# Kernel optimization log

Hardware: AMD Instinct MI355X
Metric: run time of the kernel (lower is better)

The kernel has to match this reference:

```python
import jax, jax.numpy as jnp
import numpy as np

K_RET = 10  # top-K retrieved sources per instance


def _pointnet(pts, W1, b1, W2, b2, W3, b3, Wf, bf):
    # pts: [B, P, 3] -> per-point MLP, max-pool over points, final fc -> [B, 256]
    h = jax.nn.relu(pts @ W1 + b1)
    h = jax.nn.relu(h @ W2 + b2)
    h = jax.nn.relu(h @ W3 + b3)
    g = jnp.max(h, axis=1)
    return g @ Wf + bf


def setup_inputs() -> dict:
    key = jax.random.key(0)
    ks = iter(jax.random.split(key, 48))
    B, H, W = 64, 32, 32
    S, D, PL, NPART, NPAR, PSRC = 1024, 256, 32, 16, 96, 512
    s = 0.02

    def w(shape):
        return jax.random.normal(next(ks), shape, jnp.float32) * s

    inp = {"noc_points": jax.random.normal(next(ks), (B, 3, H, W), jnp.float32)}
    # two PointNet-style encoders: target_encoder (te_) and retrieval_encoder (re_)
    for pfx in ("te", "re"):
        inp[pfx + "_W1"] = w((3, 64)); inp[pfx + "_b1"] = jnp.zeros((64,), jnp.float32)
        inp[pfx + "_W2"] = w((64, 128)); inp[pfx + "_b2"] = jnp.zeros((128,), jnp.float32)
        inp[pfx + "_W3"] = w((128, D)); inp[pfx + "_b3"] = jnp.zeros((D,), jnp.float32)
        inp[pfx + "_Wf"] = w((D, D)); inp[pfx + "_bf"] = jnp.zeros((D,), jnp.float32)
    # ParamDecoder2: input 256+256+32 = 544 -> 256 -> 256 -> 6
    inp["dec_W1"] = w((D + D + PL, 256)); inp["dec_b1"] = jnp.zeros((256,), jnp.float32)
    inp["dec_W2"] = w((256, 256)); inp["dec_b2"] = jnp.zeros((256,), jnp.float32)
    inp["dec_W3"] = w((256, 6)); inp["dec_b3"] = jnp.zeros((6,), jnp.float32)
    # precomputed source banks
    inp["ret_src_codes"] = jax.random.normal(next(ks), (S, D), jnp.float32)
    inp["src_codes"] = jax.random.normal(next(ks), (S, D), jnp.float32)
    inp["src_variances"] = jax.random.uniform(next(ks), (S, D), jnp.float32)
    inp["part_latent"] = w((S, NPART, PL))
    inp["def_param"] = w((S, NPAR))
    inp["proj_mat"] = w((S, NPAR, NPAR))        # constraint projection per source
    inp["mat"] = w((S, 3 * PSRC, NPAR))         # points_mat per source
    return inp


def reference(noc_points, te_W1, te_b1, te_W2, te_b2, te_W3, te_b3, te_Wf, te_bf,
              re_W1, re_b1, re_W2, re_b2, re_W3, re_b3, re_Wf, re_bf,
              dec_W1, dec_b1, dec_W2, dec_b2, dec_W3, dec_b3,
              ret_src_codes, src_codes, src_variances, part_latent,
              def_param, proj_mat, mat):
    B = noc_points.shape[0]
    pts = noc_points.reshape(B, 3, -1).transpose(0, 2, 1)        # [B, P, 3]
    tgt = _pointnet(pts, te_W1, te_b1, te_W2, te_b2, te_W3, te_b3, te_Wf, te_bf)  # [B, 256]
    ret = _pointnet(pts, re_W1, re_b1, re_W2, re_b2, re_W3, re_b3, re_Wf, re_bf)  # [B, 256]
    # variance-weighted squared distance to every source latent code
    d = jnp.sum(src_variances[None] * (ret[:, None, :] - ret_src_codes[None]) ** 2, axis=-1)  # [B, S]
    _, idx = jax.lax.top_k(-d, K_RET)                            # [B, K]
    NPART = part_latent.shape[1]
    src_lat = src_codes[idx]                                     # [B, K, 256]
    parts = part_latent[idx]                                     # [B, K, NPART, 32]
    tgt_b = jnp.broadcast_to(tgt[:, None, None, :], (B, K_RET, NPART, tgt.shape[-1]))
    src_b = jnp.broadcast_to(src_lat[:, :, None, :], (B, K_RET, NPART, src_lat.shape[-1]))
    x = jnp.concatenate([tgt_b, src_b, parts], axis=-1)          # [B, K, NPART, 544]
    h = jax.nn.relu(x @ dec_W1 + dec_b1)
    h = jax.nn.relu(h @ dec_W2 + dec_b2)
    raw = (h @ dec_W3 + dec_b3).reshape(B, K_RET, -1)            # [B, K, 96]
    params = jnp.einsum('bkij,bkj->bki', proj_mat[idx], raw) + def_param[idx]  # [B, K, 96]
    pts_def = jnp.einsum('bkpj,bkj->bkp', mat[idx], params)      # [B, K, 3*PSRC]
    psrc = mat.shape[1] // 3
    return pts_def.reshape(B, K_RET, psrc, 3)
```

## Files before the change

### kernel.cpp

```cpp
#include <hip/hip_runtime.h>
#include <cstdint>
#include <cstddef>


#define NB    64
#define NPTS  1024
#define NSRC  1024
#define DIM   256
#define KRET  10
#define NPART 16
#define PL    32
#define NPAR  96
#define P3    1536

__global__ __launch_bounds__(256) void pointnet_kernel(
    const float* __restrict__ noc,
    const float* __restrict__ te_W1, const float* __restrict__ te_b1,
    const float* __restrict__ te_W2, const float* __restrict__ te_b2,
    const float* __restrict__ te_W3, const float* __restrict__ te_b3,
    const float* __restrict__ re_W1, const float* __restrict__ re_b1,
    const float* __restrict__ re_W2, const float* __restrict__ re_b2,
    const float* __restrict__ re_W3, const float* __restrict__ re_b3,
    float* __restrict__ g)
{
  const int chunk = blockIdx.x;
  const int b     = blockIdx.y;
  const int e     = blockIdx.z;

  const float* W1 = e ? re_W1 : te_W1;  const float* b1 = e ? re_b1 : te_b1;
  const float* W2 = e ? re_W2 : te_W2;  const float* b2 = e ? re_b2 : te_b2;
  const float* W3 = e ? re_W3 : te_W3;  const float* b3 = e ? re_b3 : te_b3;

  __shared__ __align__(16) float h1L[64][72];
  __shared__ __align__(16) float h2L[64][132];

  const int t = threadIdx.x;

  {
    const int p = t & 63;
    const int w = t >> 6;
    const float p0 = noc[(b*3 + 0)*NPTS + chunk*64 + p];
    const float p1 = noc[(b*3 + 1)*NPTS + chunk*64 + p];
    const float p2 = noc[(b*3 + 2)*NPTS + chunk*64 + p];
    #pragma unroll
    for (int kk = 0; kk < 16; ++kk) {
      const int k = w*16 + kk;
      float v = b1[k] + p0*W1[0*64 + k] + p1*W1[1*64 + k] + p2*W1[2*64 + k];
      h1L[p][k] = fmaxf(v, 0.f);
    }
  }
  __syncthreads();

  {
    const int tp = t >> 5;
    const int tj = t & 31;
    float acc[8][4];
    #pragma unroll
    for (int pp = 0; pp < 8; ++pp)
      #pragma unroll
      for (int jj = 0; jj < 4; ++jj) acc[pp][jj] = 0.f;

    for (int k = 0; k < 64; k += 4) {
      float4 a[8];
      #pragma unroll
      for (int pp = 0; pp < 8; ++pp)
        a[pp] = *(const float4*)&h1L[tp*8 + pp][k];
      float4 w[4];
      #pragma unroll
      for (int kk = 0; kk < 4; ++kk)
        w[kk] = *(const float4*)&W2[(k + kk)*128 + tj*4];
      #pragma unroll
      for (int pp = 0; pp < 8; ++pp) {
        const float* av = (const float*)&a[pp];
        #pragma unroll
        for (int kk = 0; kk < 4; ++kk) {
          const float* wv = (const float*)&w[kk];
          #pragma unroll
          for (int jj = 0; jj < 4; ++jj)
            acc[pp][jj] += av[kk] * wv[jj];
        }
      }
    }
    float4 bv = *(const float4*)&b2[tj*4];
    const float* bvv = (const float*)&bv;
    #pragma unroll
    for (int pp = 0; pp < 8; ++pp) {
      float4 r;
      float* rv = (float*)&r;
      #pragma unroll
      for (int jj = 0; jj < 4; ++jj)
        rv[jj] = fmaxf(acc[pp][jj] + bvv[jj], 0.f);
      *(float4*)&h2L[tp*8 + pp][tj*4] = r;
    }
  }
  __syncthreads();

  {
    const int tp = t >> 5;
    const int tj = t & 31;
    float acc[8][8];
    #pragma unroll
    for (int pp = 0; pp < 8; ++pp)
      #pragma unroll
      for (int jj = 0; jj < 8; ++jj) acc[pp][jj] = 0.f;

    for (int k = 0; k < 128; k += 4) {
      float4 a[8];
      #pragma unroll
      for (int pp = 0; pp < 8; ++pp)
        a[pp] = *(const float4*)&h2L[tp*8 + pp][k];
      float4 w0[4], w1[4];
      #pragma unroll
      for (int kk = 0; kk < 4; ++kk) {
        w0[kk] = *(const float4*)&W3[(k + kk)*256 + tj*8];
        w1[kk] = *(const float4*)&W3[(k + kk)*256 + tj*8 + 4];
      }
      #pragma unroll
      for (int pp = 0; pp < 8; ++pp) {
        const float* av = (const float*)&a[pp];
        #pragma unroll
        for (int kk = 0; kk < 4; ++kk) {
          const float* wa = (const float*)&w0[kk];
          const float* wb = (const float*)&w1[kk];
          #pragma unroll
          for (int jj = 0; jj < 4; ++jj) {
            acc[pp][jj]     += av[kk] * wa[jj];
            acc[pp][jj + 4] += av[kk] * wb[jj];
          }
        }
      }
    }

    float bb[8];
    {
      float4 b3a = *(const float4*)&b3[tj*8];
      float4 b3b = *(const float4*)&b3[tj*8 + 4];
      const float* xa = (const float*)&b3a;
      const float* xb = (const float*)&b3b;
      #pragma unroll
      for (int jj = 0; jj < 4; ++jj) { bb[jj] = xa[jj]; bb[jj+4] = xb[jj]; }
    }
    float m[8];
    #pragma unroll
    for (int jj = 0; jj < 8; ++jj) {
      float mx = 0.f;
      #pragma unroll
      for (int pp = 0; pp < 8; ++pp)
        mx = fmaxf(mx, fmaxf(acc[pp][jj] + bb[jj], 0.f));
      m[jj] = mx;
    }

    float* redL = &h1L[0][0];
    {
      float4 r0, r1;
      float* a0 = (float*)&r0; float* a1 = (float*)&r1;
      #pragma unroll
      for (int jj = 0; jj < 4; ++jj) { a0[jj] = m[jj]; a1[jj] = m[jj+4]; }
      *(float4*)&redL[tp*260 + tj*8]     = r0;
      *(float4*)&redL[tp*260 + tj*8 + 4] = r1;
    }
    __syncthreads();
    {
      float mx = redL[t];
      #pragma unroll
      for (int q = 1; q < 8; ++q) mx = fmaxf(mx, redL[q*260 + t]);
      atomicMax((int*)&g[(e*NB + b)*DIM + t], __float_as_int(mx));
    }
  }
}

__global__ __launch_bounds__(256) void fc_kernel(
    const float* __restrict__ g,
    const float* __restrict__ te_Wf, const float* __restrict__ te_bf,
    const float* __restrict__ re_Wf, const float* __restrict__ re_bf,
    float* __restrict__ enc)
{
  const int be = blockIdx.x;
  const int e = be >> 6, b = be & 63;
  const float* Wf = e ? re_Wf : te_Wf;
  const float* bf = e ? re_bf : te_bf;
  __shared__ __align__(16) float gL[256];
  const int t = threadIdx.x;
  gL[t] = g[(e*NB + b)*DIM + t];
  __syncthreads();
  float acc = bf[t];
  #pragma unroll 4
  for (int i = 0; i < 256; ++i)
    acc += gL[i] * Wf[i*256 + t];
  enc[(e*NB + b)*DIM + t] = acc;
}

__global__ __launch_bounds__(256) void topk_kernel(
    const float* __restrict__ enc,
    const float* __restrict__ var,
    const float* __restrict__ codes,
    int* __restrict__ idxW)
{
  const int b = blockIdx.x;
  const int t = threadIdx.x;
  __shared__ __align__(16) float retL[256];
  __shared__ __align__(16) float dL[1024];
  __shared__ float rV[256];
  __shared__ int   rI[256];

  retL[t] = enc[(1*NB + b)*DIM + t];
  __syncthreads();

  for (int s0 = 0; s0 < 4; ++s0) {
    const int s = s0*256 + t;
    const float4* vp = (const float4*)&var[s*DIM];
    const float4* cp = (const float4*)&codes[s*DIM];
    float acc = 0.f;
    #pragma unroll 4
    for (int c = 0; c < 64; ++c) {
      float4 v  = vp[c];
      float4 cd = cp[c];
      float4 r  = *(const float4*)&retL[c*4];
      float d0 = r.x - cd.x, d1 = r.y - cd.y, d2 = r.z - cd.z, d3 = r.w - cd.w;
      acc += v.x*d0*d0 + v.y*d1*d1 + v.z*d2*d2 + v.w*d3*d3;
    }
    dL[s] = acc;
  }
  __syncthreads();

  for (int kk = 0; kk < KRET; ++kk) {
    float bv = dL[t]; int bi = t;
    #pragma unroll
    for (int s0 = 1; s0 < 4; ++s0) {
      const int s = s0*256 + t;
      const float v = dL[s];
      if (v < bv) { bv = v; bi = s; }
    }
    rV[t] = bv; rI[t] = bi;
    __syncthreads();
    for (int off = 128; off > 0; off >>= 1) {
      if (t < off) {
        const float v = rV[t + off]; const int i2 = rI[t + off];
        if (v < rV[t] || (v == rV[t] && i2 < rI[t])) { rV[t] = v; rI[t] = i2; }
      }
      __syncthreads();
    }
    if (t == 0) { idxW[b*KRET + kk] = rI[0]; dL[rI[0]] = 3.4e38f; }
    __syncthreads();
  }
}

__global__ __launch_bounds__(256) void decoder_kernel(
    const float* __restrict__ enc,
    const int*   __restrict__ idxW,
    const float* __restrict__ src_codes,
    const float* __restrict__ part_latent,
    const float* __restrict__ dW1, const float* __restrict__ db1,
    const float* __restrict__ dW2, const float* __restrict__ db2,
    const float* __restrict__ dW3, const float* __restrict__ db3,
    const float* __restrict__ def_param,
    const float* __restrict__ proj,
    const float* __restrict__ mat,
    float* __restrict__ out)
{
  const int bid = blockIdx.x;
  const int b = bid / KRET, k = bid % KRET;
  const int t = threadIdx.x;

  __shared__ __align__(16) float shx[512];
  __shared__ __align__(16) float partsL[NPART*PL];
  __shared__ __align__(16) float h1L[NPART][260];
  __shared__ __align__(16) float h2L[NPART][260];
  __shared__ __align__(16) float rawL[NPAR];
  __shared__ __align__(16) float paramsL[NPAR];

  const int s = idxW[b*KRET + k];

  shx[t]        = enc[b*DIM + t];
  shx[256 + t]  = src_codes[s*DIM + t];
  partsL[t]       = part_latent[s*512 + t];
  partsL[256 + t] = part_latent[s*512 + 256 + t];
  __syncthreads();

  {
    float acc = 0.f;
    for (int i4 = 0; i4 < 128; ++i4) {
      float4 xv = *(const float4*)&shx[i4*4];
      acc += xv.x * dW1[(i4*4 + 0)*256 + t];
      acc += xv.y * dW1[(i4*4 + 1)*256 + t];
      acc += xv.z * dW1[(i4*4 + 2)*256 + t];
      acc += xv.w * dW1[(i4*4 + 3)*256 + t];
    }
    float wreg[32];
    #pragma unroll
    for (int i = 0; i < 32; ++i) wreg[i] = dW1[(512 + i)*256 + t];
    const float base = acc + db1[t];
    #pragma unroll
    for (int n = 0; n < NPART; ++n) {
      float v = base;
      #pragma unroll
      for (int i = 0; i < 32; ++i)
        v += partsL[n*32 + i] * wreg[i];
      h1L[n][t] = fmaxf(v, 0.f);
    }
  }
  __syncthreads();

  {
    const int n  = t >> 4;
    const int jt = t & 15;
    float acc[16];
    #pragma unroll
    for (int jj = 0; jj < 16; ++jj) acc[jj] = 0.f;
    for (int c = 0; c < 256; ++c) {
      const float hv = h1L[n][c];
      const float4* wr = (const float4*)&dW2[c*256 + jt*16];
      const float4 w0 = wr[0], w1 = wr[1], w2 = wr[2], w3 = wr[3];
      acc[0]  += hv*w0.x; acc[1]  += hv*w0.y; acc[2]  += hv*w0.z; acc[3]  += hv*w0.w;
      acc[4]  += hv*w1.x; acc[5]  += hv*w1.y; acc[6]  += hv*w1.z; acc[7]  += hv*w1.w;
      acc[8]  += hv*w2.x; acc[9]  += hv*w2.y; acc[10] += hv*w2.z; acc[11] += hv*w2.w;
      acc[12] += hv*w3.x; acc[13] += hv*w3.y; acc[14] += hv*w3.z; acc[15] += hv*w3.w;
    }
    #pragma unroll
    for (int q = 0; q < 4; ++q) {
      float4 r;
      float* rv = (float*)&r;
      #pragma unroll
      for (int u = 0; u < 4; ++u) {
        const int j = jt*16 + q*4 + u;
        rv[u] = fmaxf(acc[q*4 + u] + db2[j], 0.f);
      }
      *(float4*)&h2L[n][jt*16 + q*4] = r;
    }
  }
  __syncthreads();

  if (t < 96) {
    const int n = t / 6, r = t % 6;
    float acc = db3[r];
    #pragma unroll 4
    for (int c = 0; c < 256; ++c)
      acc += h2L[n][c] * dW3[c*6 + r];
    rawL[t] = acc;
  }
  __syncthreads();

  if (t < NPAR) {
    float acc = def_param[s*NPAR + t];
    const float4* pr = (const float4*)&proj[((size_t)s*NPAR + t)*NPAR];
    #pragma unroll
    for (int j4 = 0; j4 < 24; ++j4) {
      float4 p = pr[j4];
      float4 r = *(const float4*)&rawL[j4*4];
      acc += p.x*r.x + p.y*r.y + p.z*r.z + p.w*r.w;
    }
    paramsL[t] = acc;
  }
  __syncthreads();

  for (int p = t; p < P3; p += 256) {
    const float4* mr = (const float4*)&mat[(size_t)s*P3*NPAR + (size_t)p*NPAR];
    float acc = 0.f;
    #pragma unroll
    for (int j4 = 0; j4 < 24; ++j4) {
      float4 m = mr[j4];
      float4 pa = *(const float4*)&paramsL[j4*4];
      acc += m.x*pa.x + m.y*pa.y + m.z*pa.z + m.w*pa.w;
    }
    out[((size_t)(b*KRET + k))*P3 + p] = acc;
  }
}

extern "C" void kernel_launch(void* const* d_in, const int* in_sizes, int n_in,
                              void* d_out, int out_size, void* d_ws, size_t ws_size,
                              hipStream_t stream) {
  const float* noc   = (const float*)d_in[0];
  const float* te_W1 = (const float*)d_in[1];
  const float* te_b1 = (const float*)d_in[2];
  const float* te_W2 = (const float*)d_in[3];
  const float* te_b2 = (const float*)d_in[4];
  const float* te_W3 = (const float*)d_in[5];
  const float* te_b3 = (const float*)d_in[6];
  const float* te_Wf = (const float*)d_in[7];
  const float* te_bf = (const float*)d_in[8];
  const float* re_W1 = (const float*)d_in[9];
  const float* re_b1 = (const float*)d_in[10];
  const float* re_W2 = (const float*)d_in[11];
  const float* re_b2 = (const float*)d_in[12];
  const float* re_W3 = (const float*)d_in[13];
  const float* re_b3 = (const float*)d_in[14];
  const float* re_Wf = (const float*)d_in[15];
  const float* re_bf = (const float*)d_in[16];
  const float* dec_W1 = (const float*)d_in[17];
  const float* dec_b1 = (const float*)d_in[18];
  const float* dec_W2 = (const float*)d_in[19];
  const float* dec_b2 = (const float*)d_in[20];
  const float* dec_W3 = (const float*)d_in[21];
  const float* dec_b3 = (const float*)d_in[22];
  const float* ret_src_codes = (const float*)d_in[23];
  const float* src_codes     = (const float*)d_in[24];
  const float* src_variances = (const float*)d_in[25];
  const float* part_latent   = (const float*)d_in[26];
  const float* def_param     = (const float*)d_in[27];
  const float* proj_mat      = (const float*)d_in[28];
  const float* mat           = (const float*)d_in[29];

  float* g    = (float*)d_ws;
  float* enc  = g + 2*NB*DIM;
  int*   idxW = (int*)(enc + 2*NB*DIM);

  hipMemsetAsync(d_ws, 0, 2*NB*DIM*sizeof(float), stream);

  pointnet_kernel<<<dim3(16, NB, 2), 256, 0, stream>>>(
      noc, te_W1, te_b1, te_W2, te_b2, te_W3, te_b3,
      re_W1, re_b1, re_W2, re_b2, re_W3, re_b3, g);

  fc_kernel<<<128, 256, 0, stream>>>(g, te_Wf, te_bf, re_Wf, re_bf, enc);

  topk_kernel<<<NB, 256, 0, stream>>>(enc, src_variances, ret_src_codes, idxW);

  decoder_kernel<<<640, 256, 0, stream>>>(
      enc, idxW, src_codes, part_latent,
      dec_W1, dec_b1, dec_W2, dec_b2, dec_W3, dec_b3,
      def_param, proj_mat, mat, (float*)d_out);
}
```

Measured before the change: 1.171 ms.

## Replace atomic max-pool with partial buffers, fuse fc into top-k, sort decoder blocks by source

Pointnet blocks now write per-chunk partial maxima instead of doing atomicMax, which removes the memset. The fc layer is fused into the top-k kernel, dropping one launch. A new single-block kernel counting-sorts the (batch, k) pairs by retrieved source index, so decoder blocks that share a source run close together and can reuse its proj and mat rows in cache. This costs an extra launch plus a serial single-block kernel, and the fused kernel does both fc products in only 64 blocks.

```diff
diff --git a/kernel.cpp b/kernel.cpp
--- a/kernel.cpp
+++ b/kernel.cpp
@@ -12,6 +12,7 @@
 #define PL    32
 #define NPAR  96
 #define P3    1536
+#define NCHUNK 16
 
 __global__ __launch_bounds__(256) void pointnet_kernel(
     const float* __restrict__ noc,
@@ -21,7 +22,7 @@
     const float* __restrict__ re_W1, const float* __restrict__ re_b1,
     const float* __restrict__ re_W2, const float* __restrict__ re_b2,
     const float* __restrict__ re_W3, const float* __restrict__ re_b3,
-    float* __restrict__ g)
+    float* __restrict__ g_part)
 {
   const int chunk = blockIdx.x;
   const int b     = blockIdx.y;
@@ -164,46 +165,53 @@
       float mx = redL[t];
       #pragma unroll
       for (int q = 1; q < 8; ++q) mx = fmaxf(mx, redL[q*260 + t]);
-      atomicMax((int*)&g[(e*NB + b)*DIM + t], __float_as_int(mx));
+      g_part[(((e*NB + b)*NCHUNK) + chunk)*DIM + t] = mx;
     }
   }
 }
 
-__global__ __launch_bounds__(256) void fc_kernel(
-    const float* __restrict__ g,
+__global__ __launch_bounds__(256) void fc_topk_kernel(
+    const float* __restrict__ g_part,
     const float* __restrict__ te_Wf, const float* __restrict__ te_bf,
     const float* __restrict__ re_Wf, const float* __restrict__ re_bf,
-    float* __restrict__ enc)
-{
-  const int be = blockIdx.x;
-  const int e = be >> 6, b = be & 63;
-  const float* Wf = e ? re_Wf : te_Wf;
-  const float* bf = e ? re_bf : te_bf;
-  __shared__ __align__(16) float gL[256];
-  const int t = threadIdx.x;
-  gL[t] = g[(e*NB + b)*DIM + t];
-  __syncthreads();
-  float acc = bf[t];
-  #pragma unroll 4
-  for (int i = 0; i < 256; ++i)
-    acc += gL[i] * Wf[i*256 + t];
-  enc[(e*NB + b)*DIM + t] = acc;
-}
-
-__global__ __launch_bounds__(256) void topk_kernel(
-    const float* __restrict__ enc,
     const float* __restrict__ var,
     const float* __restrict__ codes,
+    float* __restrict__ enc_te,
     int* __restrict__ idxW)
 {
   const int b = blockIdx.x;
   const int t = threadIdx.x;
+  __shared__ __align__(16) float gteL[256];
+  __shared__ __align__(16) float greL[256];
   __shared__ __align__(16) float retL[256];
   __shared__ __align__(16) float dL[1024];
   __shared__ float rV[256];
   __shared__ int   rI[256];
 
-  retL[t] = enc[(1*NB + b)*DIM + t];
+  float gte = 0.f, gre = 0.f;
+  #pragma unroll
+  for (int c = 0; c < NCHUNK; ++c) {
+    gte = fmaxf(gte, g_part[((0*NB + b)*NCHUNK + c)*DIM + t]);
+    gre = fmaxf(gre, g_part[((1*NB + b)*NCHUNK + c)*DIM + t]);
+  }
+  gteL[t] = gte;
+  greL[t] = gre;
+  __syncthreads();
+
+  {
+    float acc = te_bf[t];
+    #pragma unroll 4
+    for (int i = 0; i < 256; ++i)
+      acc += gteL[i] * te_Wf[i*256 + t];
+    enc_te[b*DIM + t] = acc;
+  }
+  {
+    float acc = re_bf[t];
+    #pragma unroll 4
+    for (int i = 0; i < 256; ++i)
+      acc += greL[i] * re_Wf[i*256 + t];
+    retL[t] = acc;
+  }
   __syncthreads();
 
   for (int s0 = 0; s0 < 4; ++s0) {
@@ -245,9 +253,52 @@
   }
 }
 
+__global__ __launch_bounds__(256) void order_kernel(
+    const int* __restrict__ idxW,
+    int* __restrict__ order)
+{
+  __shared__ int counts[NSRC];
+  __shared__ int bsum[256];
+  const int t = threadIdx.x;
+
+  #pragma unroll
+  for (int j = 0; j < 4; ++j) counts[t*4 + j] = 0;
+  __syncthreads();
+
+  for (int i = t; i < NB*KRET; i += 256)
+    atomicAdd(&counts[idxW[i]], 1);
+  __syncthreads();
+
+  const int c0 = counts[t*4 + 0], c1 = counts[t*4 + 1];
+  const int c2 = counts[t*4 + 2], c3 = counts[t*4 + 3];
+  const int local = c0 + c1 + c2 + c3;
+
+  bsum[t] = local;
+  __syncthreads();
+  for (int off = 1; off < 256; off <<= 1) {
+    const int v = (t >= off) ? bsum[t - off] : 0;
+    __syncthreads();
+    bsum[t] += v;
+    __syncthreads();
+  }
+  int run = bsum[t] - local;
+  counts[t*4 + 0] = run; run += c0;
+  counts[t*4 + 1] = run; run += c1;
+  counts[t*4 + 2] = run; run += c2;
+  counts[t*4 + 3] = run;
+  __syncthreads();
+
+  for (int i = t; i < NB*KRET; i += 256) {
+    const int s = idxW[i];
+    const int pos = atomicAdd(&counts[s], 1);
+    order[pos] = i;
+  }
+}
+
 __global__ __launch_bounds__(256) void decoder_kernel(
-    const float* __restrict__ enc,
+    const float* __restrict__ enc_te,
     const int*   __restrict__ idxW,
+    const int*   __restrict__ order,
     const float* __restrict__ src_codes,
     const float* __restrict__ part_latent,
     const float* __restrict__ dW1, const float* __restrict__ db1,
@@ -258,8 +309,8 @@
     const float* __restrict__ mat,
     float* __restrict__ out)
 {
-  const int bid = blockIdx.x;
-  const int b = bid / KRET, k = bid % KRET;
+  const int pair = order[blockIdx.x];
+  const int b = pair / KRET, k = pair % KRET;
   const int t = threadIdx.x;
 
   __shared__ __align__(16) float shx[512];
@@ -271,7 +322,7 @@
 
   const int s = idxW[b*KRET + k];
 
-  shx[t]        = enc[b*DIM + t];
+  shx[t]        = enc_te[b*DIM + t];
   shx[256 + t]  = src_codes[s*DIM + t];
   partsL[t]       = part_latent[s*512 + t];
   partsL[256 + t] = part_latent[s*512 + 256 + t];
@@ -400,22 +451,23 @@
   const float* proj_mat      = (const float*)d_in[28];
   const float* mat           = (const float*)d_in[29];
 
-  float* g    = (float*)d_ws;
-  float* enc  = g + 2*NB*DIM;
-  int*   idxW = (int*)(enc + 2*NB*DIM);
-
-  hipMemsetAsync(d_ws, 0, 2*NB*DIM*sizeof(float), stream);
-
-  pointnet_kernel<<<dim3(16, NB, 2), 256, 0, stream>>>(
+  float* g_part = (float*)d_ws;
+  float* enc_te = g_part + 2*NB*NCHUNK*DIM;
+  int*   idxW   = (int*)(enc_te + NB*DIM);
+  int*   order  = idxW + NB*KRET;
+
+  pointnet_kernel<<<dim3(NCHUNK, NB, 2), 256, 0, stream>>>(
       noc, te_W1, te_b1, te_W2, te_b2, te_W3, te_b3,
-      re_W1, re_b1, re_W2, re_b2, re_W3, re_b3, g);
-
-  fc_kernel<<<128, 256, 0, stream>>>(g, te_Wf, te_bf, re_Wf, re_bf, enc);
-
-  topk_kernel<<<NB, 256, 0, stream>>>(enc, src_variances, ret_src_codes, idxW);
+      re_W1, re_b1, re_W2, re_b2, re_W3, re_b3, g_part);
+
+  fc_topk_kernel<<<NB, 256, 0, stream>>>(
+      g_part, te_Wf, te_bf, re_Wf, re_bf,
+      src_variances, ret_src_codes, enc_te, idxW);
+
+  order_kernel<<<1, 256, 0, stream>>>(idxW, order);
 
   decoder_kernel<<<640, 256, 0, stream>>>(
-      enc, idxW, src_codes, part_latent,
+      enc_te, idxW, order, src_codes, part_latent,
       dec_W1, dec_b1, dec_W2, dec_b2, dec_W3, dec_b3,
       def_param, proj_mat, mat, (float*)d_out);
 }
```

New measurement: 1.202 ms. 1.03x slower.
